# Optimization experiments

Hardware: AMD Instinct MI355X
Metric: run time of the kernel (lower is better)

The kernel has to match this reference:

```python
import jax, jax.numpy as jnp
import numpy as np

B, DIM, H, W = 2, 384, 256, 256
HID = DIM * 1          # ffn_expansion_factor = 1 (required for source code to be consistent)
P = 8                  # patch_size


def setup_inputs() -> dict:
    key = jax.random.key(0)
    k0, k1, k2, k3, k4 = jax.random.split(key, 5)
    x = jax.random.normal(k0, (B, DIM, H, W), jnp.float32)
    # learned spectral filter: (hidden, P, P//2+1), real-valued, multiplies rfft2 coeffs
    fft_filter = jax.random.normal(k1, (HID, P, P // 2 + 1), jnp.float32)
    # project_in: 1x1 conv dim->hidden, weight (out,in)
    w_in = jax.random.normal(k2, (HID, DIM), jnp.float32) * (1.0 / np.sqrt(DIM))
    # depthwise 3x3 conv, groups=channels, weight (C,1,3,3)
    w_dw = jax.random.normal(k3, (HID, 1, 3, 3), jnp.float32) * (1.0 / 3.0)
    # project_out: 1x1 conv hidden//2 -> dim
    w_out = jax.random.normal(k4, (DIM, HID // 2), jnp.float32) * (1.0 / np.sqrt(HID // 2))
    return {"x": x, "fft_filter": fft_filter, "w_in": w_in, "w_dw": w_dw, "w_out": w_out}


def reference(x, fft_filter, w_in, w_dw, w_out):
    b, c, h, w = x.shape
    hid = w_in.shape[0]
    hb, wb = h // P, w // P
    # project_in (1x1 conv == channel GEMM)
    t = jnp.einsum('bchw,oc->bohw', x, w_in)
    # patchify into 8x8 blocks and apply per-patch 2D real FFT spectral filter.
    # reshape b c (hb p1) (wb p2) -> b c hb p1 wb p2; FFT over axes (3,5).
    tp = t.reshape(b, hid, hb, P, wb, P)
    tf = jnp.fft.rfft2(tp, axes=(3, 5))                 # (b,hid,hb,P,wb,P//2+1) complex
    tf = tf * fft_filter[None, :, None, :, None, :]
    tp = jnp.fft.irfft2(tf, s=(P, P), axes=(3, 5))
    t = tp.reshape(b, hid, h, w)
    # depthwise 3x3 conv, stride 1, padding 1
    t = jax.lax.conv_general_dilated(
        t, w_dw, window_strides=(1, 1), padding='SAME',
        feature_group_count=hid,
        dimension_numbers=('NCHW', 'OIHW', 'NCHW'))
    # gated GELU (exact erf gelu, matching torch F.gelu default)
    x1, x2 = t[:, : hid // 2], t[:, hid // 2:]
    g = jax.nn.gelu(x1, approximate=False) * x2
    # project_out (1x1 conv)
    return jnp.einsum('bchw,oc->bohw', g, w_out)
```

## Files before the change

### kernel.cpp

```cpp
#include <hip/hip_runtime.h>
#include <hip/hip_bf16.h>
#include <math.h>

#define BB 2
#define DIM 384
#define HID 384
#define HW 65536

typedef short s16x8 __attribute__((ext_vector_type(8)));
typedef short s16x4 __attribute__((ext_vector_type(4)));
typedef __bf16 bf16x8 __attribute__((ext_vector_type(8)));
typedef float f32x4 __attribute__((ext_vector_type(4)));

__device__ inline short f2b(float f) {
    __hip_bfloat16 h = __float2bfloat16(f);
    return __builtin_bit_cast(short, h);
}
__device__ inline float b2f(short s) {
    return __bfloat162float(__builtin_bit_cast(__hip_bfloat16, s));
}

__device__ inline void gl_lds16(const short* g, short* l) {
    __builtin_amdgcn_global_load_lds(
        (const __attribute__((address_space(1))) unsigned int*)g,
        (__attribute__((address_space(3))) unsigned int*)l, 16, 0, 0);
}

__global__ void k_prep(const float* __restrict__ w_in, const float* __restrict__ w_out,
                       const float* __restrict__ F,
                       short* __restrict__ wbin, short* __restrict__ wbout,
                       float* __restrict__ Dtc, short* __restrict__ Rb) {
    int i = blockIdx.x * 256 + threadIdx.x;
    if (i < 147456) { wbin[i] = f2b(w_in[i]); return; }
    i -= 147456;
    if (i < 73728) { wbout[i] = f2b(w_out[i]); return; }
    i -= 73728;
    if (i < 24576) {
        int c = i >> 6, j = i & 63;
        int a = j >> 3, q = j & 7;
        float d;
        if (q >= 1 && q <= 3)
            d = F[c * 40 + a * 5 + q];
        else if (q >= 5)
            d = F[c * 40 + ((8 - a) & 7) * 5 + (8 - q)];
        else
            d = 0.5f * (F[c * 40 + a * 5 + q] + F[c * 40 + ((8 - a) & 7) * 5 + q]);
        Dtc[i] = d * (1.f / 64.f);
        return;
    }
    i -= 24576;
    if (i < 4096) {
        int j = i >> 6, k = i & 63;
        const float cas[8] = {1.f, 1.41421356237f, 1.f, 0.f, -1.f, -1.41421356237f, -1.f, 0.f};
        int t = ((j >> 3) * (k >> 3) + (j & 7) * (k & 7)) & 7;
        Rb[i] = f2b(cas[t]);
    }
}

__global__ __launch_bounds__(256) void k_cvtx(const float* __restrict__ X, short* __restrict__ Xt) {
    int hw0 = blockIdx.x * 64, c0 = blockIdx.y * 64, b = blockIdx.z;
    __shared__ __align__(16) short S[64 * 64];
    int t = threadIdx.x;
    const float* Xb = X + ((size_t)(b * DIM) << 16);
    short* Xtb = Xt + (size_t)b * HW * DIM;
#pragma unroll
    for (int p = 0; p < 2; ++p) {
        int row = p * 32 + (t >> 3), sb = t & 7;
        const float* src = &Xb[((size_t)(c0 + row) << 16) + hw0 + sb * 8];
        float4 a = *(const float4*)src;
        float4 bq = *(const float4*)(src + 4);
        s16x8 v;
        v[0] = f2b(a.x);  v[1] = f2b(a.y);  v[2] = f2b(a.z);  v[3] = f2b(a.w);
        v[4] = f2b(bq.x); v[5] = f2b(bq.y); v[6] = f2b(bq.z); v[7] = f2b(bq.w);
        *(s16x8*)&S[row * 64 + ((sb ^ (row >> 3)) << 3)] = v;
    }
    __syncthreads();
    int h = hw0 >> 8, wb0 = hw0 & 255;
#pragma unroll
    for (int p = 0; p < 2; ++p) {
        int row = p * 32 + (t >> 3), ch = t & 7;
        s16x8 v;
#pragma unroll
        for (int j = 0; j < 8; ++j)
            v[j] = S[(ch * 8 + j) * 64 + (row ^ (ch << 3))];
        int wv = wb0 + row;
        int rowp = (((h >> 3) << 5) + (wv >> 3)) * 64 + ((h & 7) << 3) + (wv & 7);
        *(s16x8*)&Xtb[(size_t)rowp * DIM + c0 + ch * 8] = v;
    }
}

__global__ __launch_bounds__(256) void k_gemm1c(const short* __restrict__ W,
                                                const short* __restrict__ Xt,
                                                const short* __restrict__ Rb,
                                                const float* __restrict__ Dtc,
                                                short* __restrict__ T) {
    __shared__ __align__(16) short SH[17408 + 4096];
    short* Xs = SH;
    short* Ws = SH + 8192;
    short* Rs = SH + 17408;
    int d = blockIdx.x;
    int wg = (d & 7) * 192 + (d >> 3);
    int m0 = (wg % 3) * 128;
    int tx = wg / 3;
    int pid0 = tx * 2;
    int b  = blockIdx.z;
    int tid = threadIdx.x;
    int lane = tid & 63, w = tid >> 6;
    int wr = w >> 1, wc = w & 1;
    int lm = lane & 15, quad = lane >> 4;

    {
        int j0 = tid >> 3, kb0 = tid & 7;
        gl_lds16(Rb + j0 * 64 + ((kb0 ^ (j0 & 7)) << 3), Rs + tid * 8);
        int t2 = tid + 256;
        int j1 = t2 >> 3, kb1 = t2 & 7;
        gl_lds16(Rb + j1 * 64 + ((kb1 ^ (j1 & 7)) << 3), Rs + t2 * 8);
    }

    const short* Xbase = Xt + ((size_t)b * HW + (size_t)pid0 * 64) * DIM;

    f32x4 acc[4][4];
#pragma unroll
    for (int i = 0; i < 4; ++i)
#pragma unroll
        for (int j = 0; j < 4; ++j) acc[i][j] = 0.f;

    for (int kc = 0; kc < 6; ++kc) {
        int k0 = kc * 64;
#pragma unroll
        for (int q = 0; q < 4; ++q) {
            int G = q * 256 + tid;
            int row = G >> 3;
            int lg = ((G & 7) ^ (row & 7)) << 3;
            gl_lds16(Xbase + (size_t)row * DIM + k0 + lg, Xs + G * 8);
            gl_lds16(W + (size_t)(m0 + row) * DIM + k0 + lg, Ws + G * 8);
        }
        __syncthreads();
#pragma unroll
        for (int ks = 0; ks < 2; ++ks) {
            int csw = (((ks * 4 + quad) ^ (lm & 7)) << 3);
            bf16x8 af[4], bfr[4];
#pragma unroll
            for (int i = 0; i < 4; ++i)
                af[i] = __builtin_bit_cast(bf16x8, *(const s16x8*)&Xs[(wr * 64 + i * 16 + lm) * 64 + csw]);
#pragma unroll
            for (int j = 0; j < 4; ++j)
                bfr[j] = __builtin_bit_cast(bf16x8, *(const s16x8*)&Ws[(wc * 64 + j * 16 + lm) * 64 + csw]);
#pragma unroll
            for (int i = 0; i < 4; ++i)
#pragma unroll
                for (int j = 0; j < 4; ++j)
                    acc[i][j] = __builtin_amdgcn_mfma_f32_16x16x32_bf16(af[i], bfr[j], acc[i][j], 0, 0, 0);
        }
        __syncthreads();
    }

#pragma unroll
    for (int i = 0; i < 4; ++i)
#pragma unroll
        for (int j = 0; j < 4; ++j) {
            s16x4 v4;
#pragma unroll
            for (int r = 0; r < 4; ++r) v4[r] = f2b(acc[i][j][r]);
            *(s16x4*)&SH[(wc * 64 + j * 16 + lm) * 136 + wr * 64 + i * 16 + quad * 4] = v4;
        }

    f32x4 acc2[4][4];
#pragma unroll
    for (int i = 0; i < 4; ++i)
#pragma unroll
        for (int j = 0; j < 4; ++j) acc2[i][j] = 0.f;
#pragma unroll
    for (int ks = 0; ks < 2; ++ks) {
        int csw = (((ks * 4 + quad) ^ (lm & 7)) << 3);
        bf16x8 af[4], bfr[4];
#pragma unroll
        for (int i = 0; i < 4; ++i)
            af[i] = __builtin_bit_cast(bf16x8, *(const s16x8*)&Rs[(i * 16 + lm) * 64 + csw]);
#pragma unroll
        for (int j = 0; j < 4; ++j)
            bfr[j] = __builtin_bit_cast(bf16x8,
                *(const s16x8*)&SH[(wc * 64 + j * 16 + lm) * 136 + wr * 64 + ks * 32 + quad * 8]);
#pragma unroll
        for (int i = 0; i < 4; ++i)
#pragma unroll
            for (int j = 0; j < 4; ++j)
                acc2[i][j] = __builtin_amdgcn_mfma_f32_16x16x32_bf16(af[i], bfr[j], acc2[i][j], 0, 0, 0);
    }
#pragma unroll
    for (int i = 0; i < 4; ++i)
#pragma unroll
        for (int j2 = 0; j2 < 4; ++j2) {
            float4 dv = *(const float4*)&Dtc[(size_t)(m0 + wc * 64 + j2 * 16 + lm) * 64 + i * 16 + quad * 4];
            s16x4 v4;
            v4[0] = f2b(acc2[i][j2][0] * dv.x);
            v4[1] = f2b(acc2[i][j2][1] * dv.y);
            v4[2] = f2b(acc2[i][j2][2] * dv.z);
            v4[3] = f2b(acc2[i][j2][3] * dv.w);
            *(s16x4*)&SH[(wc * 64 + j2 * 16 + lm) * 136 + wr * 64 + i * 16 + quad * 4] = v4;
        }

    f32x4 acc3[4][4];
#pragma unroll
    for (int i = 0; i < 4; ++i)
#pragma unroll
        for (int j = 0; j < 4; ++j) acc3[i][j] = 0.f;
#pragma unroll
    for (int ks = 0; ks < 2; ++ks) {
        int csw = (((ks * 4 + quad) ^ (lm & 7)) << 3);
        bf16x8 af[4], bfr[4];
#pragma unroll
        for (int i = 0; i < 4; ++i)
            af[i] = __builtin_bit_cast(bf16x8, *(const s16x8*)&Rs[(i * 16 + lm) * 64 + csw]);
#pragma unroll
        for (int j = 0; j < 4; ++j)
            bfr[j] = __builtin_bit_cast(bf16x8,
                *(const s16x8*)&SH[(wc * 64 + j * 16 + lm) * 136 + wr * 64 + ks * 32 + quad * 8]);
#pragma unroll
        for (int i = 0; i < 4; ++i)
#pragma unroll
            for (int j = 0; j < 4; ++j)
                acc3[i][j] = __builtin_amdgcn_mfma_f32_16x16x32_bf16(af[i], bfr[j], acc3[i][j], 0, 0, 0);
    }
#pragma unroll
    for (int i = 0; i < 4; ++i)
#pragma unroll
        for (int j2 = 0; j2 < 4; ++j2) {
            s16x4 v4;
#pragma unroll
            for (int r = 0; r < 4; ++r) v4[r] = f2b(acc3[i][j2][r]);
            *(s16x4*)&SH[(wc * 64 + j2 * 16 + lm) * 136 + wr * 64 + i * 16 + quad * 4] = v4;
        }
    __syncthreads();
#pragma unroll
    for (int kq = 0; kq < 8; ++kq) {
        int idx = kq * 256 + tid;
        int row = idx >> 4, seg = idx & 15;
        s16x8 vv = *(const s16x8*)&SH[row * 136 + seg * 8];
        *(s16x8*)&T[(((size_t)(b * HID + m0 + row)) << 16) + pid0 * 64 + seg * 8] = vv;
    }
}

__global__ __launch_bounds__(256) void k_dwgt(const short* __restrict__ Y,
                                              const float* __restrict__ Wdw,
                                              short* __restrict__ Gt) {
    int bz = blockIdx.z;
    int b  = bz / 24;
    int cg = bz % 24;
    int c0 = cg * 8;
    int h0 = blockIdx.y * 16, w0 = blockIdx.x * 64;
    __shared__ __align__(16) short S[16][18][80];
    __shared__ float sw[16][9];
    int tid = threadIdx.x;
    if (tid < 144) {
        int p = tid / 9, j = tid % 9;
        int ch = (p < 8) ? (c0 + p) : (c0 + p - 8 + 192);
        sw[p][j] = Wdw[ch * 9 + j];
    }
    for (int t = tid; t < 2880; t += 256) {
        int v = t % 10, r = (t / 10) % 18, p = t / 180;
        int gh = h0 + r - 1;
        int gw = w0 + v * 8 - 8;
        int ch = (p < 8) ? (c0 + p) : (c0 + p - 8 + 192);
        s16x8 val = {0, 0, 0, 0, 0, 0, 0, 0};
        if (gh >= 0 && gh < 256 && gw >= 0 && gw <= 248) {
            int pid = ((gh >> 3) << 5) + (gw >> 3);
            val = *(const s16x8*)&Y[((size_t)(b * HID + ch) << 16) + (pid << 6) + ((gh & 7) << 3)];
        }
        *(s16x8*)&S[p][r][v * 8] = val;
    }
    __syncthreads();
    s16x8 ov[4];
#pragma unroll
    for (int it = 0; it < 4; ++it) {
        int idx = it * 256 + tid;
        int p = idx >> 7, run = idx & 127;
        int r = run >> 3, c8 = (run & 7) * 8;
        float z1[8], z2[8];
#pragma unroll
        for (int k = 0; k < 8; ++k) { z1[k] = 0.f; z2[k] = 0.f; }
#pragma unroll
        for (int i = 0; i < 3; ++i) {
            {
                s16x4 wv[4];
#pragma unroll
                for (int q = 0; q < 4; ++q) wv[q] = *(const s16x4*)&S[p][r + i][c8 + 4 + q * 4];
                float fv[10];
#pragma unroll
                for (int q = 0; q < 10; ++q) fv[q] = b2f(wv[(q + 3) >> 2][(q + 3) & 3]);
#pragma unroll
                for (int j = 0; j < 3; ++j) {
                    float wgt = sw[p][i * 3 + j];
#pragma unroll
                    for (int k = 0; k < 8; ++k) z1[k] += fv[k + j] * wgt;
                }
            }
            {
                s16x4 wv[4];
#pragma unroll
                for (int q = 0; q < 4; ++q) wv[q] = *(const s16x4*)&S[p + 8][r + i][c8 + 4 + q * 4];
                float fv[10];
#pragma unroll
                for (int q = 0; q < 10; ++q) fv[q] = b2f(wv[(q + 3) >> 2][(q + 3) & 3]);
#pragma unroll
                for (int j = 0; j < 3; ++j) {
                    float wgt = sw[p + 8][i * 3 + j];
#pragma unroll
                    for (int k = 0; k < 8; ++k) z2[k] += fv[k + j] * wgt;
                }
            }
        }
#pragma unroll
        for (int k = 0; k < 8; ++k) {
            float g = 0.5f * z1[k] * (1.f + erff(z1[k] * 0.70710678118654752f));
            ov[it][k] = f2b(g * z2[k]);
        }
    }
    __syncthreads();
    short* Ob = (short*)S;
#pragma unroll
    for (int it = 0; it < 4; ++it) {
        int idx = it * 256 + tid;
        int p = idx >> 7, run = idx & 127;
        int pos = (run >> 3) * 64 + (run & 7) * 8;
#pragma unroll
        for (int k = 0; k < 8; ++k)
            Ob[(pos + k) * 9 + p] = ov[it][k];
    }
    __syncthreads();
    short* Gb = Gt + (((size_t)(b * 24 + cg)) << 16) * 8;
#pragma unroll
    for (int it = 0; it < 4; ++it) {
        int pos = it * 256 + tid;
        int r = pos >> 6, cl = pos & 63;
        s16x8 v;
#pragma unroll
        for (int k = 0; k < 8; ++k) v[k] = Ob[pos * 9 + k];
        *(s16x8*)&Gb[(size_t)(((h0 + r) << 8) + w0 + cl) * 8] = v;
    }
}

__global__ __launch_bounds__(256) void k_gemm_bf16(const short* __restrict__ A,
                                                   const short* __restrict__ Bt,
                                                   float* __restrict__ C,
                                                   int N, int K) {
    __shared__ __align__(16) short SH[16384];
    const short* Bz = Bt + (size_t)blockIdx.z * (size_t)N * K;
    float* Cz = C + (size_t)blockIdx.z * (size_t)384 * N;
    int d = blockIdx.x;
    int wg = (d & 7) * 192 + (d >> 3);
    int m0 = (wg % 3) * 128;
    int n0 = (wg / 3) * 128;
    int tid = threadIdx.x;
    int lane = tid & 63, w = tid >> 6;
    int wr = w >> 1, wc = w & 1;
    int lm = lane & 15, quad = lane >> 4;

    f32x4 acc[4][4];
#pragma unroll
    for (int i = 0; i < 4; ++i)
#pragma unroll
        for (int j = 0; j < 4; ++j) acc[i][j] = 0.f;

    for (int kc = 0; kc < 3; ++kc) {
        int k0 = kc * 64;
#pragma unroll
        for (int q = 0; q < 4; ++q) {
            int G = q * 256 + tid;
            int row = G >> 3;
            int lg = (G & 7) ^ (row & 7);
            gl_lds16(A + (size_t)(m0 + row) * K + k0 + (lg << 3), SH + G * 8);
            gl_lds16(Bz + ((size_t)((k0 >> 3) + lg) * HW + n0 + row) * 8, SH + 8192 + G * 8);
        }
        __syncthreads();
#pragma unroll
        for (int ks = 0; ks < 2; ++ks) {
            int csw = (((ks * 4 + quad) ^ (lm & 7)) << 3);
            bf16x8 af[4], bfr[4];
#pragma unroll
            for (int i = 0; i < 4; ++i)
                af[i] = __builtin_bit_cast(bf16x8, *(const s16x8*)&SH[(wr * 64 + i * 16 + lm) * 64 + csw]);
#pragma unroll
            for (int j = 0; j < 4; ++j)
                bfr[j] = __builtin_bit_cast(bf16x8, *(const s16x8*)&SH[8192 + (wc * 64 + j * 16 + lm) * 64 + csw]);
#pragma unroll
            for (int i = 0; i < 4; ++i)
#pragma unroll
                for (int j = 0; j < 4; ++j)
                    acc[i][j] = __builtin_amdgcn_mfma_f32_16x16x32_bf16(af[i], bfr[j], acc[i][j], 0, 0, 0);
        }
        __syncthreads();
    }
#pragma unroll
    for (int i = 0; i < 4; ++i) {
        int r0 = m0 + wr * 64 + i * 16 + quad * 4;
#pragma unroll
        for (int j = 0; j < 4; ++j) {
            int cidx = n0 + wc * 64 + j * 16 + lm;
#pragma unroll
            for (int r = 0; r < 4; ++r)
                Cz[(size_t)(r0 + r) * N + cidx] = acc[i][j][r];
        }
    }
}

extern "C" void kernel_launch(void* const* d_in, const int* in_sizes, int n_in,
                              void* d_out, int out_size, void* d_ws, size_t ws_size,
                              hipStream_t stream) {
    const float* x     = (const float*)d_in[0];
    const float* ff    = (const float*)d_in[1];
    const float* w_in  = (const float*)d_in[2];
    const float* w_dw  = (const float*)d_in[3];
    const float* w_out = (const float*)d_in[4];
    float* out = (float*)d_out;

    char* ws = (char*)d_ws;
    float* Dtc  = (float*)ws;
    short* wbin = (short*)(ws + 98304);
    short* wbout = (short*)(ws + 393216);
    short* Rbuf = (short*)(ws + 540672);
    short* bufA = (short*)(ws + 548864);
    short* bufB = (short*)(ws + 548864 + (size_t)100663296);
    short* Gt = bufA;

    k_prep<<<976, 256, 0, stream>>>(w_in, w_out, ff, wbin, wbout, Dtc, Rbuf);

    k_cvtx<<<dim3(HW / 64, DIM / 64, BB), 256, 0, stream>>>(x, bufA);

    k_gemm1c<<<dim3(1536, 1, BB), 256, 0, stream>>>(wbin, bufA, Rbuf, Dtc, bufB);

    k_dwgt<<<dim3(4, 16, BB * 24), 256, 0, stream>>>(bufB, w_dw, Gt);

    k_gemm_bf16<<<dim3(1536, 1, BB), 256, 0, stream>>>(wbout, Gt, out, HW, 192);
}
```

Baseline: 580.2 us.

## Double-buffer LDS tiles with prefetch in both GEMM main loops

Both bf16 MFMA GEMM loops (project_in and project_out) now use a K-chunk of 32 instead of 64 and two ping-pong LDS buffers. The next chunk is issued via global_load_lds before the current chunk's MFMAs run, so global memory latency can overlap compute. This removes one barrier per iteration, but the loop runs twice as many iterations with a new XOR swizzle for the 32-wide rows. The remaining per-iteration barrier may not wait on the async LDS loads, so overlap depends on how the compiler inserts vmcnt waits.

```diff
diff --git a/kernel.cpp b/kernel.cpp
--- a/kernel.cpp
+++ b/kernel.cpp
@@ -95,8 +95,6 @@
                                                 const float* __restrict__ Dtc,
                                                 short* __restrict__ T) {
     __shared__ __align__(16) short SH[17408 + 4096];
-    short* Xs = SH;
-    short* Ws = SH + 8192;
     short* Rs = SH + 17408;
     int d = blockIdx.x;
     int wg = (d & 7) * 192 + (d >> 3);
@@ -125,33 +123,48 @@
 #pragma unroll
         for (int j = 0; j < 4; ++j) acc[i][j] = 0.f;
 
-    for (int kc = 0; kc < 6; ++kc) {
-        int k0 = kc * 64;
-#pragma unroll
-        for (int q = 0; q < 4; ++q) {
-            int G = q * 256 + tid;
-            int row = G >> 3;
-            int lg = ((G & 7) ^ (row & 7)) << 3;
-            gl_lds16(Xbase + (size_t)row * DIM + k0 + lg, Xs + G * 8);
-            gl_lds16(W + (size_t)(m0 + row) * DIM + k0 + lg, Ws + G * 8);
-        }
-        __syncthreads();
-#pragma unroll
-        for (int ks = 0; ks < 2; ++ks) {
-            int csw = (((ks * 4 + quad) ^ (lm & 7)) << 3);
-            bf16x8 af[4], bfr[4];
-#pragma unroll
-            for (int i = 0; i < 4; ++i)
-                af[i] = __builtin_bit_cast(bf16x8, *(const s16x8*)&Xs[(wr * 64 + i * 16 + lm) * 64 + csw]);
+    int grow = tid >> 2, gseg = tid & 3;
+    int gsw = (grow >> 1) & 3;
+    int gcol = ((gseg ^ gsw) << 3);
+#pragma unroll
+    for (int q = 0; q < 2; ++q) {
+        int G = q * 256 + tid;
+        int row = grow + q * 64;
+        int col = ((gseg ^ ((row >> 1) & 3)) << 3);
+        gl_lds16(Xbase + (size_t)row * DIM + col, SH + G * 8);
+        gl_lds16(W + (size_t)(m0 + row) * DIM + col, SH + 4096 + G * 8);
+    }
+    __syncthreads();
+
+    int fsw = (lm >> 1) & 3;
+    for (int kc = 0; kc < 12; ++kc) {
+        if (kc < 11) {
+            int k0 = (kc + 1) * 32;
+            int nb = ((kc + 1) & 1) * 8192;
+#pragma unroll
+            for (int q = 0; q < 2; ++q) {
+                int G = q * 256 + tid;
+                int row = grow + q * 64;
+                int col = k0 + ((gseg ^ ((row >> 1) & 3)) << 3);
+                gl_lds16(Xbase + (size_t)row * DIM + col, SH + nb + G * 8);
+                gl_lds16(W + (size_t)(m0 + row) * DIM + col, SH + nb + 4096 + G * 8);
+            }
+        }
+        const short* Xs = SH + (kc & 1) * 8192;
+        const short* Ws = Xs + 4096;
+        int csw = ((quad ^ fsw) << 3);
+        bf16x8 af[4], bfr[4];
+#pragma unroll
+        for (int i = 0; i < 4; ++i)
+            af[i] = __builtin_bit_cast(bf16x8, *(const s16x8*)&Xs[(wr * 64 + i * 16 + lm) * 32 + csw]);
+#pragma unroll
+        for (int j = 0; j < 4; ++j)
+            bfr[j] = __builtin_bit_cast(bf16x8, *(const s16x8*)&Ws[(wc * 64 + j * 16 + lm) * 32 + csw]);
+#pragma unroll
+        for (int i = 0; i < 4; ++i)
 #pragma unroll
             for (int j = 0; j < 4; ++j)
-                bfr[j] = __builtin_bit_cast(bf16x8, *(const s16x8*)&Ws[(wc * 64 + j * 16 + lm) * 64 + csw]);
-#pragma unroll
-            for (int i = 0; i < 4; ++i)
-#pragma unroll
-                for (int j = 0; j < 4; ++j)
-                    acc[i][j] = __builtin_amdgcn_mfma_f32_16x16x32_bf16(af[i], bfr[j], acc[i][j], 0, 0, 0);
-        }
+                acc[i][j] = __builtin_amdgcn_mfma_f32_16x16x32_bf16(af[i], bfr[j], acc[i][j], 0, 0, 0);
         __syncthreads();
     }
 
@@ -362,33 +375,46 @@
 #pragma unroll
         for (int j = 0; j < 4; ++j) acc[i][j] = 0.f;
 
-    for (int kc = 0; kc < 3; ++kc) {
-        int k0 = kc * 64;
-#pragma unroll
-        for (int q = 0; q < 4; ++q) {
-            int G = q * 256 + tid;
-            int row = G >> 3;
-            int lg = (G & 7) ^ (row & 7);
-            gl_lds16(A + (size_t)(m0 + row) * K + k0 + (lg << 3), SH + G * 8);
-            gl_lds16(Bz + ((size_t)((k0 >> 3) + lg) * HW + n0 + row) * 8, SH + 8192 + G * 8);
-        }
-        __syncthreads();
-#pragma unroll
-        for (int ks = 0; ks < 2; ++ks) {
-            int csw = (((ks * 4 + quad) ^ (lm & 7)) << 3);
-            bf16x8 af[4], bfr[4];
-#pragma unroll
-            for (int i = 0; i < 4; ++i)
-                af[i] = __builtin_bit_cast(bf16x8, *(const s16x8*)&SH[(wr * 64 + i * 16 + lm) * 64 + csw]);
+    int grow = tid >> 2, gseg = tid & 3;
+#pragma unroll
+    for (int q = 0; q < 2; ++q) {
+        int row = grow + q * 64;
+        int G = q * 256 + tid;
+        int sg = gseg ^ ((row >> 1) & 3);
+        gl_lds16(A + (size_t)(m0 + row) * K + (sg << 3), SH + G * 8);
+        gl_lds16(Bz + ((size_t)sg * HW + n0 + row) * 8, SH + 4096 + G * 8);
+    }
+    __syncthreads();
+
+    int fsw = (lm >> 1) & 3;
+    for (int kc = 0; kc < 6; ++kc) {
+        if (kc < 5) {
+            int k0 = (kc + 1) * 32;
+            int nb = ((kc + 1) & 1) * 8192;
+#pragma unroll
+            for (int q = 0; q < 2; ++q) {
+                int row = grow + q * 64;
+                int G = q * 256 + tid;
+                int sg = gseg ^ ((row >> 1) & 3);
+                gl_lds16(A + (size_t)(m0 + row) * K + k0 + (sg << 3), SH + nb + G * 8);
+                gl_lds16(Bz + ((size_t)((k0 >> 3) + sg) * HW + n0 + row) * 8, SH + nb + 4096 + G * 8);
+            }
+        }
+        const short* As = SH + (kc & 1) * 8192;
+        const short* Bs = As + 4096;
+        int csw = ((quad ^ fsw) << 3);
+        bf16x8 af[4], bfr[4];
+#pragma unroll
+        for (int i = 0; i < 4; ++i)
+            af[i] = __builtin_bit_cast(bf16x8, *(const s16x8*)&As[(wr * 64 + i * 16 + lm) * 32 + csw]);
+#pragma unroll
+        for (int j = 0; j < 4; ++j)
+            bfr[j] = __builtin_bit_cast(bf16x8, *(const s16x8*)&Bs[(wc * 64 + j * 16 + lm) * 32 + csw]);
+#pragma unroll
+        for (int i = 0; i < 4; ++i)
 #pragma unroll
             for (int j = 0; j < 4; ++j)
-                bfr[j] = __builtin_bit_cast(bf16x8, *(const s16x8*)&SH[8192 + (wc * 64 + j * 16 + lm) * 64 + csw]);
-#pragma unroll
-            for (int i = 0; i < 4; ++i)
-#pragma unroll
-                for (int j = 0; j < 4; ++j)
-                    acc[i][j] = __builtin_amdgcn_mfma_f32_16x16x32_bf16(af[i], bfr[j], acc[i][j], 0, 0, 0);
-        }
+                acc[i][j] = __builtin_amdgcn_mfma_f32_16x16x32_bf16(af[i], bfr[j], acc[i][j], 0, 0, 0);
         __syncthreads();
     }
 #pragma unroll
```

New measurement: 568.3 us. 2.0% less time.
